# Kernel tuning notes

Measured on AMD Instinct MI355X. Metric: run time of the kernel, lower is better.

## Reference

```python
import jax, jax.numpy as jnp
from jax import lax
import numpy as np

B, H, W, C, N = 4, 512, 512, 32, 300000
K, S, P, D = 3, 2, 1, 1  # kernel, stride, padding, dilation


def setup_inputs() -> dict:
    key = jax.random.key(0)
    kf, _ = jax.random.split(key)
    features = jax.random.normal(kf, (N, C), dtype=jnp.float32)
    # unique active coordinates (spconv requires unique sites)
    rng = np.random.default_rng(0)
    lin = rng.choice(B * H * W, size=N, replace=False)
    b = lin // (H * W)
    y = (lin // W) % H
    x = lin % W
    coors = jnp.asarray(np.stack([b, y, x], axis=1), dtype=jnp.int32)  # [N,3]
    return {"features": features, "coors": coors, "batch_size": B}


def reference(features, coors, batch_size):
    # Scatter active features onto a dense grid initialized to -inf so that
    # inputs only; outputs with no active input in window are inactive).
    neg_inf = jnp.array(-jnp.inf, dtype=features.dtype)
    dense = jnp.full((batch_size, H, W, features.shape[1]), neg_inf,
                     dtype=features.dtype)
    b, y, x = coors[:, 0], coors[:, 1], coors[:, 2]
    dense = dense.at[b, y, x].set(features)  # coords are unique
    out = lax.reduce_window(
        dense, neg_inf, lax.max,
        window_dimensions=(1, K, K, 1),
        window_strides=(1, S, S, 1),
        padding=((0, 0), (P, P), (P, P), (0, 0)),
        window_dilation=(1, D, D, 1))
    # inactive output sites -> 0 (dense view of the sparse output tensor)
    return jnp.where(jnp.isinf(out), jnp.zeros((), out.dtype), out)
```

## Files before the change

kernel.cpp:

```cpp
#include <hip/hip_runtime.h>
#include <math.h>

#define BB 4
#define HH 512
#define WW 512
#define CC 32
#define HO 256
#define WO 256

__global__ void fill_zero_kernel(int4* __restrict__ g, int n4) {
    int i = blockIdx.x * blockDim.x + threadIdx.x;
    if (i < n4) g[i] = make_int4(0, 0, 0, 0);
}

__global__ void scatter_idx_kernel(const int* __restrict__ coors,
                                   int* __restrict__ grid, int n) {
    int i = blockIdx.x * blockDim.x + threadIdx.x;
    if (i >= n) return;
    int b = coors[i * 3 + 0];
    int y = coors[i * 3 + 1];
    int x = coors[i * 3 + 2];
    grid[((size_t)b * HH + y) * WW + x] = i + 1;
}

__global__ void __launch_bounds__(256)
pool_kernel(const float4* __restrict__ feat,
            const int* __restrict__ grid,
            float4* __restrict__ out) {
    int pos = blockIdx.x * blockDim.x + threadIdx.x;
    if (pos >= BB * HO * WO) return;
    int ox = pos & (WO - 1);
    int t  = pos >> 8;
    int oy = t & (HO - 1);
    int b  = t >> 8;

    const float NEG = -INFINITY;
    float4 acc[8];
#pragma unroll
    for (int j = 0; j < 8; ++j) acc[j] = make_float4(NEG, NEG, NEG, NEG);

    int iy0 = 2 * oy - 1;
    int ix0 = 2 * ox - 1;
#pragma unroll
    for (int dy = 0; dy < 3; ++dy) {
        int iy = iy0 + dy;
        if (iy < 0 || iy >= HH) continue;
        const int* grow = grid + ((size_t)b * HH + iy) * WW;
#pragma unroll
        for (int dx = 0; dx < 3; ++dx) {
            int ix = ix0 + dx;
            if (ix < 0 || ix >= WW) continue;
            int idx = grow[ix];
            if (idx == 0) continue;
            const float4* f = feat + (size_t)(idx - 1) * 8;
#pragma unroll
            for (int j = 0; j < 8; ++j) {
                float4 v = f[j];
                acc[j].x = fmaxf(acc[j].x, v.x);
                acc[j].y = fmaxf(acc[j].y, v.y);
                acc[j].z = fmaxf(acc[j].z, v.z);
                acc[j].w = fmaxf(acc[j].w, v.w);
            }
        }
    }

    float4* o = out + (size_t)pos * 8;
#pragma unroll
    for (int j = 0; j < 8; ++j) {
        float4 v = acc[j];
        v.x = isinf(v.x) ? 0.0f : v.x;
        v.y = isinf(v.y) ? 0.0f : v.y;
        v.z = isinf(v.z) ? 0.0f : v.z;
        v.w = isinf(v.w) ? 0.0f : v.w;
        o[j] = v;
    }
}

extern "C" void kernel_launch(void* const* d_in, const int* in_sizes, int n_in,
                              void* d_out, int out_size, void* d_ws, size_t ws_size,
                              hipStream_t stream) {
    const float* features = (const float*)d_in[0];
    const int*   coors    = (const int*)d_in[1];
    int n = in_sizes[0] / CC;

    int* grid = (int*)d_ws;

    {
        int n4 = (BB * HH * WW) / 4;
        int blk = 256, grd = (n4 + blk - 1) / blk;
        fill_zero_kernel<<<grd, blk, 0, stream>>>((int4*)grid, n4);
    }
    {
        int blk = 256, grd = (n + blk - 1) / blk;
        scatter_idx_kernel<<<grd, blk, 0, stream>>>(coors, grid, n);
    }
    {
        int npos = BB * HO * WO;
        int blk = 256, grd = (npos + blk - 1) / blk;
        pool_kernel<<<grd, blk, 0, stream>>>((const float4*)features, grid,
                                             (float4*)d_out);
    }
}
```

Baseline: 113.6 us.

## Split each output site across 8 threads, one float4 channel group each

The pool kernel now assigns one thread per (output site, 4-channel group) instead of one thread per output site. Each group of 8 consecutive threads reads a contiguous 128-byte feature row and writes a contiguous output row, so global loads and stores coalesce, and each thread needs only one accumulator instead of eight. In exchange, the grid index loads and bounds checks are repeated 8 times per site, and the grid is launched with 8x as many threads.

```diff
diff --git a/kernel.cpp b/kernel.cpp
--- a/kernel.cpp
+++ b/kernel.cpp
@@ -27,53 +27,47 @@
 pool_kernel(const float4* __restrict__ feat,
             const int* __restrict__ grid,
             float4* __restrict__ out) {
-    int pos = blockIdx.x * blockDim.x + threadIdx.x;
-    if (pos >= BB * HO * WO) return;
+    int tid = blockIdx.x * blockDim.x + threadIdx.x;
+    int cg  = tid & 7;
+    int pos = tid >> 3;
+
     int ox = pos & (WO - 1);
     int t  = pos >> 8;
     int oy = t & (HO - 1);
     int b  = t >> 8;
 
     const float NEG = -INFINITY;
-    float4 acc[8];
-#pragma unroll
-    for (int j = 0; j < 8; ++j) acc[j] = make_float4(NEG, NEG, NEG, NEG);
+    float4 acc = make_float4(NEG, NEG, NEG, NEG);
 
     int iy0 = 2 * oy - 1;
     int ix0 = 2 * ox - 1;
+    const int* gb = grid + (size_t)b * (HH * WW);
+
 #pragma unroll
     for (int dy = 0; dy < 3; ++dy) {
         int iy = iy0 + dy;
-        if (iy < 0 || iy >= HH) continue;
-        const int* grow = grid + ((size_t)b * HH + iy) * WW;
+        if ((unsigned)iy >= (unsigned)HH) continue;
+        const int* grow = gb + iy * WW;
 #pragma unroll
         for (int dx = 0; dx < 3; ++dx) {
             int ix = ix0 + dx;
-            if (ix < 0 || ix >= WW) continue;
+            if ((unsigned)ix >= (unsigned)WW) continue;
             int idx = grow[ix];
-            if (idx == 0) continue;
-            const float4* f = feat + (size_t)(idx - 1) * 8;
-#pragma unroll
-            for (int j = 0; j < 8; ++j) {
-                float4 v = f[j];
-                acc[j].x = fmaxf(acc[j].x, v.x);
-                acc[j].y = fmaxf(acc[j].y, v.y);
-                acc[j].z = fmaxf(acc[j].z, v.z);
-                acc[j].w = fmaxf(acc[j].w, v.w);
+            if (idx != 0) {
+                float4 v = feat[(size_t)(idx - 1) * 8 + cg];
+                acc.x = fmaxf(acc.x, v.x);
+                acc.y = fmaxf(acc.y, v.y);
+                acc.z = fmaxf(acc.z, v.z);
+                acc.w = fmaxf(acc.w, v.w);
             }
         }
     }
 
-    float4* o = out + (size_t)pos * 8;
-#pragma unroll
-    for (int j = 0; j < 8; ++j) {
-        float4 v = acc[j];
-        v.x = isinf(v.x) ? 0.0f : v.x;
-        v.y = isinf(v.y) ? 0.0f : v.y;
-        v.z = isinf(v.z) ? 0.0f : v.z;
-        v.w = isinf(v.w) ? 0.0f : v.w;
-        o[j] = v;
-    }
+    acc.x = isinf(acc.x) ? 0.0f : acc.x;
+    acc.y = isinf(acc.y) ? 0.0f : acc.y;
+    acc.z = isinf(acc.z) ? 0.0f : acc.z;
+    acc.w = isinf(acc.w) ? 0.0f : acc.w;
+    out[(size_t)pos * 8 + cg] = acc;
 }
 
 extern "C" void kernel_launch(void* const* d_in, const int* in_sizes, int n_in,
@@ -95,8 +89,8 @@
         scatter_idx_kernel<<<grd, blk, 0, stream>>>(coors, grid, n);
     }
     {
-        int npos = BB * HO * WO;
-        int blk = 256, grd = (npos + blk - 1) / blk;
+        int nthreads = BB * HO * WO * 8;
+        int blk = 256, grd = nthreads / blk;
         pool_kernel<<<grd, blk, 0, stream>>>((const float4*)features, grid,
                                              (float4*)d_out);
     }
```

Measured after the change: 122.5 us. +7.9%, slower.
